# Performance work log

Hardware: AMD Instinct MI355X
Metric: run time of the kernel (lower is better)

## Reference

```python
import jax, jax.numpy as jnp
import numpy as np

D_LATENT = 128
WIDTH = 64
MODES = 32
N_LAYERS = 4
N_INST = 8
LIFT_L = 64   # lift_shape = (width, 64)
B = 128
OUT_LEN = 4096
EPS = 1e-5


def _gelu(x):
    return jax.nn.gelu(x, approximate=False)  # torch nn.GELU default = exact erf


def setup_inputs() -> dict:
    key = jax.random.key(0)
    ks = jax.random.split(key, 16)
    n = lambda k, shape, s=0.02: (s * jax.random.normal(k, shape)).astype(jnp.float32)
    spec_scale = 1.0 / (WIDTH * WIDTH)
    return {
        "z": jax.random.normal(ks[0], (B, D_LATENT), dtype=jnp.float32),
        "instrument_params": jax.random.normal(ks[1], (B, N_INST), dtype=jnp.float32),
        "lift_w": n(ks[2], (D_LATENT, WIDTH * LIFT_L)),
        "lift_b": jnp.zeros((WIDTH * LIFT_L,), jnp.float32),
        "inst_w1": n(ks[3], (N_INST, WIDTH), 0.3),
        "inst_b1": jnp.zeros((WIDTH,), jnp.float32),
        "inst_w2": n(ks[4], (WIDTH, WIDTH), 0.1),
        "inst_b2": jnp.zeros((WIDTH,), jnp.float32),
        "spec_w": (spec_scale * jax.random.normal(ks[5], (N_LAYERS, WIDTH, WIDTH, MODES, 2))).astype(jnp.float32),
        "pw_w": n(ks[6], (N_LAYERS, WIDTH, WIDTH), 0.1),   # (layer, out, in)
        "pw_b": jnp.zeros((N_LAYERS, WIDTH), jnp.float32),
        "proj_w1": n(ks[7], (2 * WIDTH, WIDTH), 0.1),      # (out, in)
        "proj_b1": jnp.zeros((2 * WIDTH,), jnp.float32),
        "proj_w2": n(ks[8], (1, 2 * WIDTH), 0.1),
        "proj_b2": jnp.zeros((1,), jnp.float32),
        "out_len": OUT_LEN,
    }


def _interp_linear(x, out_len):
    # torch F.interpolate(mode='linear', align_corners=False)
    in_len = x.shape[-1]
    src = jnp.clip((jnp.arange(out_len, dtype=x.dtype) + 0.5) * (in_len / out_len) - 0.5, 0.0, in_len - 1)
    i0 = jnp.floor(src).astype(jnp.int32)
    i1 = jnp.minimum(i0 + 1, in_len - 1)
    w = src - i0.astype(x.dtype)
    return x[..., i0] * (1.0 - w) + x[..., i1] * w


def _spectral_conv(x, w):
    # x: (B, C, L) real; w: (C_in, C_out, modes, 2)
    L = x.shape[-1]
    xf = jnp.fft.rfft(x, axis=-1)                 # (B, C, L//2+1) complex64
    xr = jnp.real(xf[:, :, :MODES])
    xi = jnp.imag(xf[:, :, :MODES])
    wr, wi = w[..., 0], w[..., 1]
    out_r = jnp.einsum('bim,iom->bom', xr, wr) - jnp.einsum('bim,iom->bom', xi, wi)
    out_i = jnp.einsum('bim,iom->bom', xr, wi) + jnp.einsum('bim,iom->bom', xi, wr)
    n_freq = L // 2 + 1
    of = (out_r + 1j * out_i).astype(xf.dtype)
    of = jnp.pad(of, ((0, 0), (0, 0), (0, n_freq - MODES)))
    return jnp.fft.irfft(of, n=L, axis=-1)


def reference(z, instrument_params, lift_w, lift_b, inst_w1, inst_b1, inst_w2, inst_b2,
              spec_w, pw_w, pw_b, proj_w1, proj_b1, proj_w2, proj_b2, out_len):
    Bz = z.shape[0]
    x = (z @ lift_w + lift_b).reshape(Bz, WIDTH, LIFT_L)
    x = _interp_linear(x, out_len)                              # (B, W, L)
    cond = _gelu(instrument_params @ inst_w1 + inst_b1) @ inst_w2 + inst_b2
    x = x + cond[:, :, None]
    for l in range(N_LAYERS):
        x1 = _spectral_conv(x, spec_w[l])
        x2 = jnp.einsum('bil,oi->bol', x, pw_w[l]) + pw_b[l][None, :, None]
        h = x1 + x2
        mu = h.mean(axis=-1, keepdims=True)
        var = h.var(axis=-1, keepdims=True)                     # biased, like InstanceNorm1d
        x = _gelu((h - mu) * jax.lax.rsqrt(var + EPS))
    h = _gelu(jnp.einsum('bil,oi->bol', x, proj_w1) + proj_b1[None, :, None])
    out = jnp.einsum('bil,oi->bol', h, proj_w2) + proj_b2[None, :, None]
    return out[:, 0, :]                                         # (B, out_len)
```

## Files before the change

### kernel.cpp

```cpp
#include <hip/hip_runtime.h>
#include <math.h>


typedef _Float16 half8 __attribute__((ext_vector_type(8)));
typedef __attribute__((ext_vector_type(4))) float fx4;

__device__ __forceinline__ float gelu_f(float x){
    float u = x*x;
    float a = x * fmaf(-0.1029443f, u, -2.3022083f);
    float e = exp2f(a);
    float r = __builtin_amdgcn_rcpf(1.0f + e);
    return x * r;
}
__device__ __forceinline__ unsigned short f2h(float f){
    union { _Float16 h; unsigned short u; } c;
    c.h = (_Float16)f;
    return c.u;
}
__device__ __forceinline__ float h2f(unsigned short u){
    union { unsigned short u; _Float16 h; } c;
    c.u = u;
    return (float)c.h;
}

static const size_t OFF_XH    = 0;
static const size_t OFF_XT    = 16777216;
static const size_t OFF_TABB  = 33554432;
static const size_t OFF_TABT  = 33685504;
static const size_t OFF_MAH   = 33816576;
static const size_t OFF_PWWH  = 34078720;
static const size_t OFF_W1H   = 34086912;
static const size_t OFF_COND  = 34091008;
static const size_t OFF_STATS = 34099200;
static const size_t OFF_DFTP  = 34115584;
static const size_t OFF_X0    = 38309888;

__global__ void k_tab(unsigned short* __restrict__ tabB, unsigned short* __restrict__ tabT,
                      const float* __restrict__ pww, unsigned short* __restrict__ pwwh,
                      const float* __restrict__ pj1w, unsigned short* __restrict__ w1h){
    int t = blockIdx.x*256 + threadIdx.x;
    if (t < 16384) pwwh[t] = f2h(pww[t]);
    if (t < 8192)  w1h[t]  = f2h(pj1w[t]);
    int m2 = t >> 12, n = t & 4095;
    int m = m2 & 31;
    int r = (m*n) & 4095;
    int r2 = (r >= 2048) ? (r - 4096) : r;
    float a = (float)r2 * 1.5339807878856412e-3f;
    float v = (m2 >= 32) ? sinf(a) : cosf(a);
    tabB[(size_t)m2*4096 + n] = f2h(v);
    tabT[(size_t)n*64 + m2]   = f2h(v * 0.015625f);
}

__global__ __launch_bounds__(64) void k_cond(const float* __restrict__ instp,
        const float* __restrict__ w1, const float* __restrict__ b1,
        const float* __restrict__ w2, const float* __restrict__ b2,
        float* __restrict__ cond){
    int b = blockIdx.x, tid = threadIdx.x;
    __shared__ float ipl[8];
    __shared__ float tl[64];
    if (tid < 8) ipl[tid] = instp[b*8 + tid];
    __syncthreads();
    float s = b1[tid];
    #pragma unroll
    for (int k = 0; k < 8; ++k) s = fmaf(ipl[k], w1[k*64 + tid], s);
    tl[tid] = gelu_f(s);
    __syncthreads();
    float c = b2[tid];
    #pragma unroll 8
    for (int j = 0; j < 64; ++j) c = fmaf(tl[j], w2[j*64 + tid], c);
    cond[b*64 + tid] = c;
}

__global__ __launch_bounds__(256) void k_liftc(const float* __restrict__ z,
        const float* __restrict__ lw, const float* __restrict__ lb,
        const float* __restrict__ cond, float* __restrict__ x0){
    int b = blockIdx.x, q = blockIdx.y;
    int t = threadIdx.x;
    __shared__ float zl[128];
    if (t < 128) zl[t] = z[b*128 + t];
    __syncthreads();
    #pragma unroll
    for (int i = 0; i < 4; ++i){
        int e = q*1024 + i*256 + t;
        float s = lb[e];
        #pragma unroll 8
        for (int d = 0; d < 128; ++d)
            s = fmaf(zl[d], lw[(size_t)d*4096 + e], s);
        x0[(size_t)b*4096 + e] = s + cond[b*64 + (e >> 6)];
    }
}

template<int MODE, int DODFT>
__global__ __launch_bounds__(256) void k_prep(
        const unsigned short* __restrict__ xhp, const float* __restrict__ statsr,
        const unsigned short* __restrict__ tabB, const float* __restrict__ x0,
        unsigned short* __restrict__ xT, float* __restrict__ dftp)
{
    int b = blockIdx.x, ng = blockIdx.y;
    int t = threadIdx.x;
    int w = t >> 6, lane = t & 63;
    int lrow = lane & 15, g = lane >> 4;
    __shared__ __align__(16) unsigned short xl[2][4096];
    __shared__ float xs[(MODE == 2) ? 65*64 : 1];
    int co = t >> 2, nq = t & 3;
    float mu = 0.f, rs = 1.f;
    if (MODE == 1){
        float2 sr = *(const float2*)(statsr + (size_t)(b*64+co)*2);
        mu = sr.x * (1.f/4096.f);
        float var = fmaf(sr.y, 1.f/4096.f, -mu*mu);
        rs = rsqrtf(var + 1e-5f);
    }
    if (MODE == 2){
        const float* xb0 = x0 + (size_t)b*4096;
        #pragma unroll
        for (int i = 0; i < 16; ++i){
            int idx = i*256 + t;
            xs[(idx >> 6)*65 + (idx & 63)] = xb0[idx];
        }
        __syncthreads();
    }
    fx4 acc[4];
    #pragma unroll
    for (int i = 0; i < 4; ++i) acc[i] = (fx4){0.f,0.f,0.f,0.f};

    const unsigned short* hrow = xhp + ((size_t)(b*64+co))*4096 + ng*512 + nq*16;
    unsigned short* xtbase = xT + ((size_t)b*4096 + (size_t)ng*512)*64;

    uint4 cA, cB;
    if (MODE == 1){ cA = *(const uint4*)(hrow); cB = *(const uint4*)(hrow + 8); }
    for (int it = 0; it < 8; ++it){
        int n0 = ng*512 + it*64;
        char* xb = (char*)(&xl[it & 1][0]);
        uint4 nA, nB;
        if (MODE == 1 && it < 7){
            nA = *(const uint4*)(hrow + (it+1)*64);
            nB = *(const uint4*)(hrow + (it+1)*64 + 8);
        }
        unsigned int pk[8];
        if (MODE == 1){
            unsigned int hu[8] = {cA.x,cA.y,cA.z,cA.w,cB.x,cB.y,cB.z,cB.w};
            #pragma unroll
            for (int i = 0; i < 8; ++i){
                float f0 = h2f((unsigned short)(hu[i] & 0xFFFFu));
                float f1 = h2f((unsigned short)(hu[i] >> 16));
                f0 = gelu_f((f0 - mu)*rs);
                f1 = gelu_f((f1 - mu)*rs);
                pk[i] = (unsigned int)f2h(f0) | ((unsigned int)f2h(f1) << 16);
            }
        } else {
            const float* xr = xs + co*65;
            #pragma unroll
            for (int i = 0; i < 8; ++i){
                float v[2];
                #pragma unroll
                for (int q = 0; q < 2; ++q){
                    int n = n0 + nq*16 + i*2 + q;
                    float src = (n + 0.5f)*0.015625f - 0.5f;
                    src = fminf(fmaxf(src, 0.0f), 63.0f);
                    int i0 = (int)src;
                    int i1 = (i0 + 1 > 63) ? 63 : (i0 + 1);
                    float wt = src - (float)i0;
                    v[q] = xr[i0] + wt*(xr[i1] - xr[i0]);
                }
                pk[i] = (unsigned int)f2h(v[0]) | ((unsigned int)f2h(v[1]) << 16);
            }
        }
        unsigned int base = (unsigned int)co*128 + (unsigned int)nq*32;
        unsigned int sw = (unsigned int)((co & 7) << 4);
        *(uint4*)(xb + ((base +  0) ^ sw)) = make_uint4(pk[0],pk[1],pk[2],pk[3]);
        *(uint4*)(xb + ((base + 16) ^ sw)) = make_uint4(pk[4],pk[5],pk[6],pk[7]);
        __syncthreads();

        if (DODFT){
            int m0 = w*16;
            #pragma unroll
            for (int ks = 0; ks < 2; ++ks){
                int kk = ks*32 + g*8;
                half8 af = *(const half8*)(tabB + (size_t)(m0 + lrow)*4096 + n0 + kk);
                #pragma unroll
                for (int ct = 0; ct < 4; ++ct){
                    int row = ct*16 + lrow;
                    unsigned int ba = ((unsigned int)row*128 + (unsigned int)kk*2)
                                      ^ (unsigned int)((row & 7) << 4);
                    half8 bf = *(const half8*)(xb + ba);
                    acc[ct] = __builtin_amdgcn_mfma_f32_16x16x32_f16(af, bf, acc[ct], 0, 0, 0);
                }
            }
        }
        {
            int n = t & 63, coq = t >> 6;
            unsigned int opk[8];
            #pragma unroll
            for (int i = 0; i < 8; ++i){
                int r0 = coq*16 + 2*i, r1 = r0 + 1;
                unsigned int a0 = ((unsigned int)r0*128 + (unsigned int)n*2)
                                  ^ (unsigned int)((r0 & 7) << 4);
                unsigned int a1 = ((unsigned int)r1*128 + (unsigned int)n*2)
                                  ^ (unsigned int)((r1 & 7) << 4);
                unsigned short v0 = *(const unsigned short*)(xb + a0);
                unsigned short v1 = *(const unsigned short*)(xb + a1);
                opk[i] = (unsigned int)v0 | ((unsigned int)v1 << 16);
            }
            unsigned short* dst = xtbase + (size_t)(it*64 + n)*64 + coq*16;
            *(uint4*)dst       = make_uint4(opk[0],opk[1],opk[2],opk[3]);
            *(uint4*)(dst + 8) = make_uint4(opk[4],opk[5],opk[6],opk[7]);
        }
        if (MODE == 1 && it < 7){ cA = nA; cB = nB; }
    }
    if (DODFT){
        int m0 = w*16;
        #pragma unroll
        for (int ct = 0; ct < 4; ++ct){
            float4 v = make_float4(acc[ct][0], acc[ct][1], acc[ct][2], acc[ct][3]);
            *(float4*)(dftp + ((size_t)(b*8+ng)*64 + ct*16 + lrow)*64 + m0 + g*4) = v;
        }
    }
}

__global__ __launch_bounds__(256) void k_mix(const float* __restrict__ dftp,
        const float* __restrict__ specw, unsigned short* __restrict__ mah,
        float* __restrict__ statsr, int l){
    int b = blockIdx.x, coq = blockIdx.y, t = threadIdx.x;
    __shared__ float xm[64*64];
    if (t < 128) statsr[b*128 + t] = 0.f;
    const float* dp = dftp + (size_t)b*8*4096;
    #pragma unroll
    for (int i = 0; i < 4; ++i){
        int e = i*1024 + t*4;
        float4 s = make_float4(0.f,0.f,0.f,0.f);
        #pragma unroll
        for (int ng = 0; ng < 8; ++ng){
            float4 v = *(const float4*)(dp + (size_t)ng*4096 + e);
            s.x += v.x; s.y += v.y; s.z += v.z; s.w += v.w;
        }
        if (e & 32){ s.x = -s.x; s.y = -s.y; s.z = -s.z; s.w = -s.w; }
        *(float4*)(xm + e) = s;
    }
    __syncthreads();
    int mq = t & 3, ciq = (t >> 2) & 3, co_l = t >> 4;
    int co = coq*16 + co_l;
    float yr[8] = {0,0,0,0,0,0,0,0}, yi[8] = {0,0,0,0,0,0,0,0};
    const float* wbase = specw + (size_t)l*262144 + (size_t)co*64 + mq*16;
    #pragma unroll 4
    for (int cil = 0; cil < 16; ++cil){
        int ci = ciq*16 + cil;
        const float* wp = wbase + (size_t)ci*4096;
        float4 w0 = *(const float4*)(wp);
        float4 w1v = *(const float4*)(wp + 4);
        float4 w2v = *(const float4*)(wp + 8);
        float4 w3v = *(const float4*)(wp + 12);
        const float* xc = xm + ci*64 + mq*8;
        float4 r0 = *(const float4*)(xc);
        float4 r1 = *(const float4*)(xc + 4);
        float4 i0 = *(const float4*)(xc + 32);
        float4 i1 = *(const float4*)(xc + 36);
        float wr[8] = {w0.x,w0.z,w1v.x,w1v.z,w2v.x,w2v.z,w3v.x,w3v.z};
        float wi[8] = {w0.y,w0.w,w1v.y,w1v.w,w2v.y,w2v.w,w3v.y,w3v.w};
        float xr[8] = {r0.x,r0.y,r0.z,r0.w,r1.x,r1.y,r1.z,r1.w};
        float xi[8] = {i0.x,i0.y,i0.z,i0.w,i1.x,i1.y,i1.z,i1.w};
        #pragma unroll
        for (int mm = 0; mm < 8; ++mm){
            yr[mm] = fmaf(xr[mm], wr[mm], fmaf(-xi[mm], wi[mm], yr[mm]));
            yi[mm] = fmaf(xr[mm], wi[mm], fmaf( xi[mm], wr[mm], yi[mm]));
        }
    }
    #pragma unroll
    for (int mm = 0; mm < 8; ++mm){
        yr[mm] += __shfl_xor(yr[mm], 4); yr[mm] += __shfl_xor(yr[mm], 8);
        yi[mm] += __shfl_xor(yi[mm], 4); yi[mm] += __shfl_xor(yi[mm], 8);
    }
    if (ciq == 0){
        unsigned short* mb = mah + (size_t)(b*64 + co)*64;
        unsigned int pr[4], pi[4];
        #pragma unroll
        for (int p = 0; p < 4; ++p){
            int m0 = mq*8 + 2*p;
            float s0 = (m0 == 0) ? 0.015625f : 0.03125f;
            pr[p] = (unsigned int)f2h(s0*yr[2*p]) | ((unsigned int)f2h(0.03125f*yr[2*p+1]) << 16);
            pi[p] = (unsigned int)f2h(-0.03125f*yi[2*p]) | ((unsigned int)f2h(-0.03125f*yi[2*p+1]) << 16);
        }
        *(uint4*)(mb + mq*8)      = make_uint4(pr[0],pr[1],pr[2],pr[3]);
        *(uint4*)(mb + 32 + mq*8) = make_uint4(pi[0],pi[1],pi[2],pi[3]);
    }
}

__global__ __launch_bounds__(256, 4) void k_pass3(
        const unsigned short* __restrict__ xT, const unsigned short* __restrict__ tabT,
        const unsigned short* __restrict__ pwwh, const float* __restrict__ pwb,
        const unsigned short* __restrict__ mah, unsigned short* __restrict__ xh,
        float* __restrict__ statsr, int lay)
{
    int b = blockIdx.x, ntg = blockIdx.y;
    int t = threadIdx.x, w = t >> 6, lane = t & 63;
    int lrow = lane & 15, g = lane >> 4;
    int nsl = ntg*256 + w*64;

    half8 A[4][4];
    #pragma unroll
    for (int nt = 0; nt < 4; ++nt){
        int n = nsl + nt*16 + lrow;
        #pragma unroll
        for (int ks = 0; ks < 4; ++ks){
            int k = ks*32 + g*8;
            const unsigned short* src = (k < 64)
                ? (xT   + ((size_t)b*4096 + n)*64 + k)
                : (tabT + (size_t)n*64 + (k - 64));
            A[nt][ks] = *(const half8*)src;
        }
    }
    __shared__ float sred[2][4][64];
    #pragma unroll
    for (int cot = 0; cot < 4; ++cot){
        int co = cot*16 + lrow;
        half8 Bv[4];
        #pragma unroll
        for (int ks = 0; ks < 4; ++ks){
            int k = ks*32 + g*8;
            const unsigned short* src = (k < 64)
                ? (pwwh + ((size_t)lay*64 + co)*64 + k)
                : (mah  + ((size_t)b*64 + co)*64 + (k - 64));
            Bv[ks] = *(const half8*)src;
        }
        fx4 acc[4];
        #pragma unroll
        for (int i = 0; i < 4; ++i) acc[i] = (fx4){0.f,0.f,0.f,0.f};
        #pragma unroll
        for (int ks = 0; ks < 4; ++ks)
            #pragma unroll
            for (int nt = 0; nt < 4; ++nt)
                acc[nt] = __builtin_amdgcn_mfma_f32_16x16x32_f16(A[nt][ks], Bv[ks], acc[nt], 0, 0, 0);

        float pb = pwb[lay*64 + co];
        unsigned short* hr = xh + ((size_t)(b*64+co))*4096;
        float sS = 0.f, sQ = 0.f;
        #pragma unroll
        for (int nt = 0; nt < 4; ++nt){
            float h0 = acc[nt][0] + pb;
            float h1 = acc[nt][1] + pb;
            float h2 = acc[nt][2] + pb;
            float h3 = acc[nt][3] + pb;
            uint2 pk;
            pk.x = (unsigned int)f2h(h0) | ((unsigned int)f2h(h1) << 16);
            pk.y = (unsigned int)f2h(h2) | ((unsigned int)f2h(h3) << 16);
            *(uint2*)(hr + nsl + nt*16 + g*4) = pk;
            sS += (h0 + h1) + (h2 + h3);
            float q = h0*h0;
            q = fmaf(h1, h1, q); q = fmaf(h2, h2, q); q = fmaf(h3, h3, q);
            sQ += q;
        }
        sS += __shfl_xor(sS, 16); sQ += __shfl_xor(sQ, 16);
        sS += __shfl_xor(sS, 32); sQ += __shfl_xor(sQ, 32);
        if (g == 0){
            sred[0][w][cot*16 + lrow] = sS;
            sred[1][w][cot*16 + lrow] = sQ;
        }
    }
    __syncthreads();
    if (t < 64){
        float S = 0.f, Q = 0.f;
        #pragma unroll
        for (int ww = 0; ww < 4; ++ww){ S += sred[0][ww][t]; Q += sred[1][ww][t]; }
        atomicAdd(statsr + (size_t)(b*64+t)*2,     S);
        atomicAdd(statsr + (size_t)(b*64+t)*2 + 1, Q);
    }
}

__global__ __launch_bounds__(256) void k_proj2(
        const unsigned short* __restrict__ xhp, const float* __restrict__ statsr,
        const unsigned short* __restrict__ w1h, const float* __restrict__ b1,
        const float* __restrict__ w2, const float* __restrict__ b2,
        float* __restrict__ out)
{
    int b = blockIdx.x, ng = blockIdx.y;
    int t = threadIdx.x, w = t >> 6, lane = t & 63;
    int lrow = lane & 15, g = lane >> 4;
    int o2h = w & 1, nhalf = w >> 1;
    __shared__ __align__(16) unsigned short xl[2][4096];
    __shared__ float sred[2][2][2][2][16];

    int ci = t >> 2, nq = t & 3;
    float2 sr = *(const float2*)(statsr + (size_t)(b*64+ci)*2);
    float mu = sr.x * (1.f/4096.f);
    float var = fmaf(sr.y, 1.f/4096.f, -mu*mu);
    float rs = rsqrtf(var + 1e-5f);
    const unsigned short* hrow = xhp + ((size_t)(b*64+ci))*4096 + ng*512 + nq*16;

    half8 A[4][2];
    #pragma unroll
    for (int ot = 0; ot < 4; ++ot)
        #pragma unroll
        for (int ks = 0; ks < 2; ++ks)
            A[ot][ks] = *(const half8*)(w1h + (size_t)(o2h*64 + ot*16 + lrow)*64 + ks*32 + g*8);
    float bb[16], wv[16];
    #pragma unroll
    for (int ot = 0; ot < 4; ++ot)
        #pragma unroll
        for (int j = 0; j < 4; ++j){
            int o2 = o2h*64 + ot*16 + g*4 + j;
            bb[ot*4+j] = b1[o2];
            wv[ot*4+j] = w2[o2];
        }
    float bias2 = b2[0];

    uint4 cA = *(const uint4*)(hrow);
    uint4 cB = *(const uint4*)(hrow + 8);
    for (int it = 0; it < 8; ++it){
        char* xb = (char*)(&xl[it & 1][0]);
        uint4 nA, nB;
        if (it < 7){
            nA = *(const uint4*)(hrow + (it+1)*64);
            nB = *(const uint4*)(hrow + (it+1)*64 + 8);
        }
        unsigned int pk[8];
        {
            unsigned int hu[8] = {cA.x,cA.y,cA.z,cA.w,cB.x,cB.y,cB.z,cB.w};
            #pragma unroll
            for (int i = 0; i < 8; ++i){
                float f0 = h2f((unsigned short)(hu[i] & 0xFFFFu));
                float f1 = h2f((unsigned short)(hu[i] >> 16));
                f0 = gelu_f((f0 - mu)*rs);
                f1 = gelu_f((f1 - mu)*rs);
                pk[i] = (unsigned int)f2h(f0) | ((unsigned int)f2h(f1) << 16);
            }
        }
        unsigned int base = (unsigned int)ci*128 + (unsigned int)nq*32;
        unsigned int sw = (unsigned int)((ci & 7) << 4);
        *(uint4*)(xb + ((base +  0) ^ sw)) = make_uint4(pk[0],pk[1],pk[2],pk[3]);
        *(uint4*)(xb + ((base + 16) ^ sw)) = make_uint4(pk[4],pk[5],pk[6],pk[7]);
        __syncthreads();

        if (it > 0 && t < 64){
            int nh = t >> 5, rem = t & 31, ntf = rem >> 4, cl = rem & 15;
            out[(size_t)b*4096 + ng*512 + (it-1)*64 + t] =
                sred[(it-1)&1][nh][ntf][0][cl] + sred[(it-1)&1][nh][ntf][1][cl] + bias2;
        }

        #pragma unroll
        for (int nt = 0; nt < 2; ++nt){
            int n_l = nhalf*32 + nt*16 + lrow;
            half8 Bf[2];
            #pragma unroll
            for (int ks = 0; ks < 2; ++ks){
                union { unsigned short u[8]; half8 v; } bu;
                #pragma unroll
                for (int e = 0; e < 8; ++e){
                    int cie = ks*32 + g*8 + e;
                    unsigned int ba = ((unsigned int)cie*128 + (unsigned int)n_l*2)
                                      ^ (unsigned int)((cie & 7) << 4);
                    bu.u[e] = *(const unsigned short*)(xb + ba);
                }
                Bf[ks] = bu.v;
            }
            fx4 acc[4];
            #pragma unroll
            for (int i = 0; i < 4; ++i) acc[i] = (fx4){0.f,0.f,0.f,0.f};
            #pragma unroll
            for (int ks = 0; ks < 2; ++ks)
                #pragma unroll
                for (int ot = 0; ot < 4; ++ot)
                    acc[ot] = __builtin_amdgcn_mfma_f32_16x16x32_f16(A[ot][ks], Bf[ks], acc[ot], 0, 0, 0);
            float p = 0.f;
            #pragma unroll
            for (int ot = 0; ot < 4; ++ot)
                #pragma unroll
                for (int j = 0; j < 4; ++j)
                    p = fmaf(wv[ot*4+j], gelu_f(acc[ot][j] + bb[ot*4+j]), p);
            p += __shfl_xor(p, 16); p += __shfl_xor(p, 32);
            if (lane < 16) sred[it & 1][nhalf][nt][o2h][lane] = p;
        }
        if (it < 7){ cA = nA; cB = nB; }
    }
    __syncthreads();
    if (t < 64){
        int nh = t >> 5, rem = t & 31, ntf = rem >> 4, cl = rem & 15;
        out[(size_t)b*4096 + ng*512 + 7*64 + t] =
            sred[1][nh][ntf][0][cl] + sred[1][nh][ntf][1][cl] + bias2;
    }
}

extern "C" void kernel_launch(void* const* d_in, const int* in_sizes, int n_in,
                              void* d_out, int out_size, void* d_ws, size_t ws_size,
                              hipStream_t stream) {
    (void)in_sizes; (void)n_in; (void)out_size; (void)ws_size;
    const float* z      = (const float*)d_in[0];
    const float* instp  = (const float*)d_in[1];
    const float* lift_w = (const float*)d_in[2];
    const float* lift_b = (const float*)d_in[3];
    const float* iw1    = (const float*)d_in[4];
    const float* ib1    = (const float*)d_in[5];
    const float* iw2    = (const float*)d_in[6];
    const float* ib2    = (const float*)d_in[7];
    const float* specw  = (const float*)d_in[8];
    const float* pww    = (const float*)d_in[9];
    const float* pwb    = (const float*)d_in[10];
    const float* pj1w   = (const float*)d_in[11];
    const float* pj1b   = (const float*)d_in[12];
    const float* pj2w   = (const float*)d_in[13];
    const float* pj2b   = (const float*)d_in[14];

    float* ws = (float*)d_ws;
    unsigned short* xh    = (unsigned short*)(ws + OFF_XH);
    unsigned short* xT    = (unsigned short*)(ws + OFF_XT);
    unsigned short* tabB  = (unsigned short*)(ws + OFF_TABB);
    unsigned short* tabT  = (unsigned short*)(ws + OFF_TABT);
    unsigned short* mah   = (unsigned short*)(ws + OFF_MAH);
    unsigned short* pwwh  = (unsigned short*)(ws + OFF_PWWH);
    unsigned short* w1h   = (unsigned short*)(ws + OFF_W1H);
    float* cond   = ws + OFF_COND;
    float* statsr = ws + OFF_STATS;
    float* dftp   = ws + OFF_DFTP;
    float* x0     = ws + OFF_X0;
    float* out    = (float*)d_out;

    k_tab  <<<dim3(1024),  dim3(256), 0, stream>>>(tabB, tabT, pww, pwwh, pj1w, w1h);
    k_cond <<<dim3(128),   dim3(64),  0, stream>>>(instp, iw1, ib1, iw2, ib2, cond);
    k_liftc<<<dim3(128,4), dim3(256), 0, stream>>>(z, lift_w, lift_b, cond, x0);

    for (int l = 0; l < 4; ++l){
        if (l == 0)
            k_prep<2,1><<<dim3(128,8), dim3(256), 0, stream>>>(xh, statsr, tabB, x0, xT, dftp);
        else
            k_prep<1,1><<<dim3(128,8), dim3(256), 0, stream>>>(xh, statsr, tabB, x0, xT, dftp);
        k_mix  <<<dim3(128,4),  dim3(256), 0, stream>>>(dftp, specw, mah, statsr, l);
        k_pass3<<<dim3(128,16), dim3(256), 0, stream>>>(xT, tabT, pwwh, pwb, mah, xh, statsr, l);
    }
    k_proj2<<<dim3(128,8), dim3(256), 0, stream>>>(xh, statsr, w1h, pj1b, pj2w, pj2b, out);
}
```

Baseline: 442.3 us.

## Recompute normalized activations in pass3 instead of storing transposed xT buffer

The prep kernel no longer writes a transposed fp16 copy of the activations (xT). The pointwise/inverse-DFT kernel now reads the raw pre-norm activations itself, applies instance norm and GELU (or the lift interpolation on layer 0), and transposes through LDS before the MFMA. Stats are double-buffered so pass3 can read the previous layer's stats while accumulating new ones. The projection kernel also gets an LDS transpose so its B fragments load as vectors instead of scalar gathers. This removes a large global write and read per layer, at the cost of redundant GELU work, extra barriers, fewer blocks (grid 16→8 in y) and lower occupancy hints.

Result: faster. 420.1 us, median of 2 (-5.0%).

```diff
diff --git a/kernel.cpp b/kernel.cpp
--- a/kernel.cpp
+++ b/kernel.cpp
@@ -23,17 +23,17 @@
     return (float)c.h;
 }
 
-static const size_t OFF_XH    = 0;
-static const size_t OFF_XT    = 16777216;
-static const size_t OFF_TABB  = 33554432;
-static const size_t OFF_TABT  = 33685504;
-static const size_t OFF_MAH   = 33816576;
-static const size_t OFF_PWWH  = 34078720;
-static const size_t OFF_W1H   = 34086912;
-static const size_t OFF_COND  = 34091008;
-static const size_t OFF_STATS = 34099200;
-static const size_t OFF_DFTP  = 34115584;
-static const size_t OFF_X0    = 38309888;
+static const size_t OFF_XH     = 0;
+static const size_t OFF_TABB   = 33554432;
+static const size_t OFF_TABT   = 33685504;
+static const size_t OFF_MAH    = 33816576;
+static const size_t OFF_PWWH   = 34078720;
+static const size_t OFF_W1H    = 34086912;
+static const size_t OFF_COND   = 34091008;
+static const size_t OFF_STATS  = 34099200;
+static const size_t OFF_DFTP   = 34115584;
+static const size_t OFF_X0     = 38309888;
+static const size_t OFF_STATS2 = 38834176;
 
 __global__ void k_tab(unsigned short* __restrict__ tabB, unsigned short* __restrict__ tabT,
                       const float* __restrict__ pww, unsigned short* __restrict__ pwwh,
@@ -90,11 +90,11 @@
     }
 }
 
-template<int MODE, int DODFT>
+template<int MODE>
 __global__ __launch_bounds__(256) void k_prep(
-        const unsigned short* __restrict__ xhp, const float* __restrict__ statsr,
+        const unsigned short* __restrict__ xhp, const float* __restrict__ statsIn,
         const unsigned short* __restrict__ tabB, const float* __restrict__ x0,
-        unsigned short* __restrict__ xT, float* __restrict__ dftp)
+        float* __restrict__ dftp)
 {
     int b = blockIdx.x, ng = blockIdx.y;
     int t = threadIdx.x;
@@ -102,10 +102,10 @@
     int lrow = lane & 15, g = lane >> 4;
     __shared__ __align__(16) unsigned short xl[2][4096];
     __shared__ float xs[(MODE == 2) ? 65*64 : 1];
-    int co = t >> 2, nq = t & 3;
+    int ci = t >> 2, nq = t & 3;
     float mu = 0.f, rs = 1.f;
     if (MODE == 1){
-        float2 sr = *(const float2*)(statsr + (size_t)(b*64+co)*2);
+        float2 sr = *(const float2*)(statsIn + (size_t)(b*64+ci)*2);
         mu = sr.x * (1.f/4096.f);
         float var = fmaf(sr.y, 1.f/4096.f, -mu*mu);
         rs = rsqrtf(var + 1e-5f);
@@ -123,8 +123,7 @@
     #pragma unroll
     for (int i = 0; i < 4; ++i) acc[i] = (fx4){0.f,0.f,0.f,0.f};
 
-    const unsigned short* hrow = xhp + ((size_t)(b*64+co))*4096 + ng*512 + nq*16;
-    unsigned short* xtbase = xT + ((size_t)b*4096 + (size_t)ng*512)*64;
+    const unsigned short* hrow = xhp + ((size_t)(b*64+ci))*4096 + ng*512 + nq*16;
 
     uint4 cA, cB;
     if (MODE == 1){ cA = *(const uint4*)(hrow); cB = *(const uint4*)(hrow + 8); }
@@ -148,7 +147,7 @@
                 pk[i] = (unsigned int)f2h(f0) | ((unsigned int)f2h(f1) << 16);
             }
         } else {
-            const float* xr = xs + co*65;
+            const float* xr = xs + ci*65;
             #pragma unroll
             for (int i = 0; i < 8; ++i){
                 float v[2];
@@ -165,13 +164,13 @@
                 pk[i] = (unsigned int)f2h(v[0]) | ((unsigned int)f2h(v[1]) << 16);
             }
         }
-        unsigned int base = (unsigned int)co*128 + (unsigned int)nq*32;
-        unsigned int sw = (unsigned int)((co & 7) << 4);
+        unsigned int base = (unsigned int)ci*128 + (unsigned int)nq*32;
+        unsigned int sw = (unsigned int)((ci & 7) << 4);
         *(uint4*)(xb + ((base +  0) ^ sw)) = make_uint4(pk[0],pk[1],pk[2],pk[3]);
         *(uint4*)(xb + ((base + 16) ^ sw)) = make_uint4(pk[4],pk[5],pk[6],pk[7]);
         __syncthreads();
 
-        if (DODFT){
+        {
             int m0 = w*16;
             #pragma unroll
             for (int ks = 0; ks < 2; ++ks){
@@ -187,27 +186,9 @@
                 }
             }
         }
-        {
-            int n = t & 63, coq = t >> 6;
-            unsigned int opk[8];
-            #pragma unroll
-            for (int i = 0; i < 8; ++i){
-                int r0 = coq*16 + 2*i, r1 = r0 + 1;
-                unsigned int a0 = ((unsigned int)r0*128 + (unsigned int)n*2)
-                                  ^ (unsigned int)((r0 & 7) << 4);
-                unsigned int a1 = ((unsigned int)r1*128 + (unsigned int)n*2)
-                                  ^ (unsigned int)((r1 & 7) << 4);
-                unsigned short v0 = *(const unsigned short*)(xb + a0);
-                unsigned short v1 = *(const unsigned short*)(xb + a1);
-                opk[i] = (unsigned int)v0 | ((unsigned int)v1 << 16);
-            }
-            unsigned short* dst = xtbase + (size_t)(it*64 + n)*64 + coq*16;
-            *(uint4*)dst       = make_uint4(opk[0],opk[1],opk[2],opk[3]);
-            *(uint4*)(dst + 8) = make_uint4(opk[4],opk[5],opk[6],opk[7]);
-        }
         if (MODE == 1 && it < 7){ cA = nA; cB = nB; }
     }
-    if (DODFT){
+    {
         int m0 = w*16;
         #pragma unroll
         for (int ct = 0; ct < 4; ++ct){
@@ -219,10 +200,10 @@
 
 __global__ __launch_bounds__(256) void k_mix(const float* __restrict__ dftp,
         const float* __restrict__ specw, unsigned short* __restrict__ mah,
-        float* __restrict__ statsr, int l){
+        float* __restrict__ statsZero, int l){
     int b = blockIdx.x, coq = blockIdx.y, t = threadIdx.x;
     __shared__ float xm[64*64];
-    if (t < 128) statsr[b*128 + t] = 0.f;
+    if (t < 128) statsZero[b*128 + t] = 0.f;
     const float* dp = dftp + (size_t)b*8*4096;
     #pragma unroll
     for (int i = 0; i < 4; ++i){
@@ -284,42 +265,133 @@
     }
 }
 
-__global__ __launch_bounds__(256, 4) void k_pass3(
-        const unsigned short* __restrict__ xT, const unsigned short* __restrict__ tabT,
+template<int MODE>
+__global__ __launch_bounds__(256, 2) void k_pass3(
+        const unsigned short* __restrict__ xhp, const float* __restrict__ statsIn,
+        const float* __restrict__ x0, const unsigned short* __restrict__ tabT,
         const unsigned short* __restrict__ pwwh, const float* __restrict__ pwb,
         const unsigned short* __restrict__ mah, unsigned short* __restrict__ xh,
-        float* __restrict__ statsr, int lay)
+        float* __restrict__ statsOut, int lay)
 {
-    int b = blockIdx.x, ntg = blockIdx.y;
+    int b = blockIdx.x, ng = blockIdx.y;
     int t = threadIdx.x, w = t >> 6, lane = t & 63;
     int lrow = lane & 15, g = lane >> 4;
-    int nsl = ntg*256 + w*64;
-
-    half8 A[4][4];
-    #pragma unroll
-    for (int nt = 0; nt < 4; ++nt){
-        int n = nsl + nt*16 + lrow;
-        #pragma unroll
-        for (int ks = 0; ks < 4; ++ks){
-            int k = ks*32 + g*8;
-            const unsigned short* src = (k < 64)
-                ? (xT   + ((size_t)b*4096 + n)*64 + k)
-                : (tabT + (size_t)n*64 + (k - 64));
-            A[nt][ks] = *(const half8*)src;
-        }
-    }
+    __shared__ __align__(16) unsigned short xl1[4096];
+    __shared__ __align__(16) unsigned short xl2[4096];
+    __shared__ float xs[(MODE == 2) ? 65*64 : 1];
     __shared__ float sred[2][4][64];
+
+    int ci = t >> 2, nq = t & 3;
+    float mu = 0.f, rs = 1.f;
+    if (MODE == 1){
+        float2 sr = *(const float2*)(statsIn + (size_t)(b*64+ci)*2);
+        mu = sr.x * (1.f/4096.f);
+        float var = fmaf(sr.y, 1.f/4096.f, -mu*mu);
+        rs = rsqrtf(var + 1e-5f);
+    }
+    if (MODE == 2){
+        const float* xb0 = x0 + (size_t)b*4096;
+        #pragma unroll
+        for (int i = 0; i < 16; ++i){
+            int idx = i*256 + t;
+            xs[(idx >> 6)*65 + (idx & 63)] = xb0[idx];
+        }
+        __syncthreads();
+    }
+    half8 Bv[4][4];
     #pragma unroll
     for (int cot = 0; cot < 4; ++cot){
         int co = cot*16 + lrow;
-        half8 Bv[4];
         #pragma unroll
         for (int ks = 0; ks < 4; ++ks){
             int k = ks*32 + g*8;
             const unsigned short* src = (k < 64)
                 ? (pwwh + ((size_t)lay*64 + co)*64 + k)
                 : (mah  + ((size_t)b*64 + co)*64 + (k - 64));
-            Bv[ks] = *(const half8*)src;
+            Bv[cot][ks] = *(const half8*)src;
+        }
+    }
+    float pb[4];
+    #pragma unroll
+    for (int cot = 0; cot < 4; ++cot) pb[cot] = pwb[lay*64 + cot*16 + lrow];
+    float sS[4] = {0,0,0,0}, sQ[4] = {0,0,0,0};
+
+    const unsigned short* hrow = xhp + ((size_t)(b*64+ci))*4096 + ng*512 + nq*16;
+    uint4 cA, cB;
+    if (MODE == 1){ cA = *(const uint4*)(hrow); cB = *(const uint4*)(hrow + 8); }
+
+    for (int it = 0; it < 8; ++it){
+        int n0 = ng*512 + it*64;
+        uint4 nA, nB;
+        if (MODE == 1 && it < 7){
+            nA = *(const uint4*)(hrow + (it+1)*64);
+            nB = *(const uint4*)(hrow + (it+1)*64 + 8);
+        }
+        unsigned int pk[8];
+        if (MODE == 1){
+            unsigned int hu[8] = {cA.x,cA.y,cA.z,cA.w,cB.x,cB.y,cB.z,cB.w};
+            #pragma unroll
+            for (int i = 0; i < 8; ++i){
+                float f0 = h2f((unsigned short)(hu[i] & 0xFFFFu));
+                float f1 = h2f((unsigned short)(hu[i] >> 16));
+                f0 = gelu_f((f0 - mu)*rs);
+                f1 = gelu_f((f1 - mu)*rs);
+                pk[i] = (unsigned int)f2h(f0) | ((unsigned int)f2h(f1) << 16);
+            }
+        } else {
+            const float* xr = xs + ci*65;
+            #pragma unroll
+            for (int i = 0; i < 8; ++i){
+                float v[2];
+                #pragma unroll
+                for (int q = 0; q < 2; ++q){
+                    int n = n0 + nq*16 + i*2 + q;
+                    float src = (n + 0.5f)*0.015625f - 0.5f;
+                    src = fminf(fmaxf(src, 0.0f), 63.0f);
+                    int i0 = (int)src;
+                    int i1 = (i0 + 1 > 63) ? 63 : (i0 + 1);
+                    float wt = src - (float)i0;
+                    v[q] = xr[i0] + wt*(xr[i1] - xr[i0]);
+                }
+                pk[i] = (unsigned int)f2h(v[0]) | ((unsigned int)f2h(v[1]) << 16);
+            }
+        }
+        unsigned int base = (unsigned int)ci*128 + (unsigned int)nq*32;
+        unsigned int sw = (unsigned int)((ci & 7) << 4);
+        *(uint4*)((char*)xl1 + ((base +  0) ^ sw)) = make_uint4(pk[0],pk[1],pk[2],pk[3]);
+        *(uint4*)((char*)xl1 + ((base + 16) ^ sw)) = make_uint4(pk[4],pk[5],pk[6],pk[7]);
+        __syncthreads();
+
+        {
+            int n = t & 63, coq = t >> 6;
+            unsigned int opk[8];
+            #pragma unroll
+            for (int i = 0; i < 8; ++i){
+                int r0 = coq*16 + 2*i, r1 = r0 + 1;
+                unsigned int a0 = ((unsigned int)r0*128 + (unsigned int)n*2)
+                                  ^ (unsigned int)((r0 & 7) << 4);
+                unsigned int a1 = ((unsigned int)r1*128 + (unsigned int)n*2)
+                                  ^ (unsigned int)((r1 & 7) << 4);
+                unsigned short v0 = *(const unsigned short*)((const char*)xl1 + a0);
+                unsigned short v1 = *(const unsigned short*)((const char*)xl1 + a1);
+                opk[i] = (unsigned int)v0 | ((unsigned int)v1 << 16);
+            }
+            unsigned int b0 = (unsigned int)n*128 + (unsigned int)coq*32;
+            unsigned int swn = (unsigned int)((n & 7) << 4);
+            *(uint4*)((char*)xl2 + ((b0 +  0) ^ swn)) = make_uint4(opk[0],opk[1],opk[2],opk[3]);
+            *(uint4*)((char*)xl2 + ((b0 + 16) ^ swn)) = make_uint4(opk[4],opk[5],opk[6],opk[7]);
+        }
+        __syncthreads();
+
+        int nl = w*16 + lrow;
+        unsigned int swa = (unsigned int)((nl & 7) << 4);
+        half8 Af[4];
+        Af[0] = *(const half8*)((const char*)xl2 + (((unsigned int)nl*128 +  0 + g*16) ^ swa));
+        Af[1] = *(const half8*)((const char*)xl2 + (((unsigned int)nl*128 + 64 + g*16) ^ swa));
+        {
+            const unsigned short* tb = tabT + (size_t)(n0 + nl)*64 + g*8;
+            Af[2] = *(const half8*)(tb);
+            Af[3] = *(const half8*)(tb + 32);
         }
         fx4 acc[4];
         #pragma unroll
@@ -327,32 +399,36 @@
         #pragma unroll
         for (int ks = 0; ks < 4; ++ks)
             #pragma unroll
-            for (int nt = 0; nt < 4; ++nt)
-                acc[nt] = __builtin_amdgcn_mfma_f32_16x16x32_f16(A[nt][ks], Bv[ks], acc[nt], 0, 0, 0);
-
-        float pb = pwb[lay*64 + co];
-        unsigned short* hr = xh + ((size_t)(b*64+co))*4096;
-        float sS = 0.f, sQ = 0.f;
-        #pragma unroll
-        for (int nt = 0; nt < 4; ++nt){
-            float h0 = acc[nt][0] + pb;
-            float h1 = acc[nt][1] + pb;
-            float h2 = acc[nt][2] + pb;
-            float h3 = acc[nt][3] + pb;
-            uint2 pk;
-            pk.x = (unsigned int)f2h(h0) | ((unsigned int)f2h(h1) << 16);
-            pk.y = (unsigned int)f2h(h2) | ((unsigned int)f2h(h3) << 16);
-            *(uint2*)(hr + nsl + nt*16 + g*4) = pk;
-            sS += (h0 + h1) + (h2 + h3);
+            for (int cot = 0; cot < 4; ++cot)
+                acc[cot] = __builtin_amdgcn_mfma_f32_16x16x32_f16(Af[ks], Bv[cot][ks], acc[cot], 0, 0, 0);
+
+        #pragma unroll
+        for (int cot = 0; cot < 4; ++cot){
+            int co = cot*16 + lrow;
+            unsigned short* hr = xh + ((size_t)(b*64+co))*4096;
+            float h0 = acc[cot][0] + pb[cot];
+            float h1 = acc[cot][1] + pb[cot];
+            float h2 = acc[cot][2] + pb[cot];
+            float h3 = acc[cot][3] + pb[cot];
+            uint2 pk2;
+            pk2.x = (unsigned int)f2h(h0) | ((unsigned int)f2h(h1) << 16);
+            pk2.y = (unsigned int)f2h(h2) | ((unsigned int)f2h(h3) << 16);
+            *(uint2*)(hr + n0 + w*16 + g*4) = pk2;
+            sS[cot] += (h0 + h1) + (h2 + h3);
             float q = h0*h0;
             q = fmaf(h1, h1, q); q = fmaf(h2, h2, q); q = fmaf(h3, h3, q);
-            sQ += q;
-        }
-        sS += __shfl_xor(sS, 16); sQ += __shfl_xor(sQ, 16);
-        sS += __shfl_xor(sS, 32); sQ += __shfl_xor(sQ, 32);
+            sQ[cot] += q;
+        }
+        if (MODE == 1 && it < 7){ cA = nA; cB = nB; }
+    }
+    #pragma unroll
+    for (int cot = 0; cot < 4; ++cot){
+        float s = sS[cot], q = sQ[cot];
+        s += __shfl_xor(s, 16); q += __shfl_xor(q, 16);
+        s += __shfl_xor(s, 32); q += __shfl_xor(q, 32);
         if (g == 0){
-            sred[0][w][cot*16 + lrow] = sS;
-            sred[1][w][cot*16 + lrow] = sQ;
+            sred[0][w][cot*16 + lrow] = s;
+            sred[1][w][cot*16 + lrow] = q;
         }
     }
     __syncthreads();
@@ -360,13 +436,13 @@
         float S = 0.f, Q = 0.f;
         #pragma unroll
         for (int ww = 0; ww < 4; ++ww){ S += sred[0][ww][t]; Q += sred[1][ww][t]; }
-        atomicAdd(statsr + (size_t)(b*64+t)*2,     S);
-        atomicAdd(statsr + (size_t)(b*64+t)*2 + 1, Q);
+        atomicAdd(statsOut + (size_t)(b*64+t)*2,     S);
+        atomicAdd(statsOut + (size_t)(b*64+t)*2 + 1, Q);
     }
 }
 
 __global__ __launch_bounds__(256) void k_proj2(
-        const unsigned short* __restrict__ xhp, const float* __restrict__ statsr,
+        const unsigned short* __restrict__ xhp, const float* __restrict__ statsIn,
         const unsigned short* __restrict__ w1h, const float* __restrict__ b1,
         const float* __restrict__ w2, const float* __restrict__ b2,
         float* __restrict__ out)
@@ -375,11 +451,12 @@
     int t = threadIdx.x, w = t >> 6, lane = t & 63;
     int lrow = lane & 15, g = lane >> 4;
     int o2h = w & 1, nhalf = w >> 1;
-    __shared__ __align__(16) unsigned short xl[2][4096];
+    __shared__ __align__(16) unsigned short xl1[4096];
+    __shared__ __align__(16) unsigned short xl2[4096];
     __shared__ float sred[2][2][2][2][16];
 
     int ci = t >> 2, nq = t & 3;
-    float2 sr = *(const float2*)(statsr + (size_t)(b*64+ci)*2);
+    float2 sr = *(const float2*)(statsIn + (size_t)(b*64+ci)*2);
     float mu = sr.x * (1.f/4096.f);
     float var = fmaf(sr.y, 1.f/4096.f, -mu*mu);
     float rs = rsqrtf(var + 1e-5f);
@@ -405,7 +482,6 @@
     uint4 cA = *(const uint4*)(hrow);
     uint4 cB = *(const uint4*)(hrow + 8);
     for (int it = 0; it < 8; ++it){
-        char* xb = (char*)(&xl[it & 1][0]);
         uint4 nA, nB;
         if (it < 7){
             nA = *(const uint4*)(hrow + (it+1)*64);
@@ -425,8 +501,29 @@
         }
         unsigned int base = (unsigned int)ci*128 + (unsigned int)nq*32;
         unsigned int sw = (unsigned int)((ci & 7) << 4);
-        *(uint4*)(xb + ((base +  0) ^ sw)) = make_uint4(pk[0],pk[1],pk[2],pk[3]);
-        *(uint4*)(xb + ((base + 16) ^ sw)) = make_uint4(pk[4],pk[5],pk[6],pk[7]);
+        *(uint4*)((char*)xl1 + ((base +  0) ^ sw)) = make_uint4(pk[0],pk[1],pk[2],pk[3]);
+        *(uint4*)((char*)xl1 + ((base + 16) ^ sw)) = make_uint4(pk[4],pk[5],pk[6],pk[7]);
+        __syncthreads();
+
+        {
+            int n = t & 63, coq = t >> 6;
+            unsigned int opk[8];
+            #pragma unroll
+            for (int i = 0; i < 8; ++i){
+                int r0 = coq*16 + 2*i, r1 = r0 + 1;
+                unsigned int a0 = ((unsigned int)r0*128 + (unsigned int)n*2)
+                                  ^ (unsigned int)((r0 & 7) << 4);
+                unsigned int a1 = ((unsigned int)r1*128 + (unsigned int)n*2)
+                                  ^ (unsigned int)((r1 & 7) << 4);
+                unsigned short v0 = *(const unsigned short*)((const char*)xl1 + a0);
+                unsigned short v1 = *(const unsigned short*)((const char*)xl1 + a1);
+                opk[i] = (unsigned int)v0 | ((unsigned int)v1 << 16);
+            }
+            unsigned int b0 = (unsigned int)n*128 + (unsigned int)coq*32;
+            unsigned int swn = (unsigned int)((n & 7) << 4);
+            *(uint4*)((char*)xl2 + ((b0 +  0) ^ swn)) = make_uint4(opk[0],opk[1],opk[2],opk[3]);
+            *(uint4*)((char*)xl2 + ((b0 + 16) ^ swn)) = make_uint4(opk[4],opk[5],opk[6],opk[7]);
+        }
         __syncthreads();
 
         if (it > 0 && t < 64){
@@ -438,19 +535,10 @@
         #pragma unroll
         for (int nt = 0; nt < 2; ++nt){
             int n_l = nhalf*32 + nt*16 + lrow;
+            unsigned int swa = (unsigned int)((n_l & 7) << 4);
             half8 Bf[2];
-            #pragma unroll
-            for (int ks = 0; ks < 2; ++ks){
-                union { unsigned short u[8]; half8 v; } bu;
-                #pragma unroll
-                for (int e = 0; e < 8; ++e){
-                    int cie = ks*32 + g*8 + e;
-                    unsigned int ba = ((unsigned int)cie*128 + (unsigned int)n_l*2)
-                                      ^ (unsigned int)((cie & 7) << 4);
-                    bu.u[e] = *(const unsigned short*)(xb + ba);
-                }
-                Bf[ks] = bu.v;
-            }
+            Bf[0] = *(const half8*)((const char*)xl2 + (((unsigned int)n_l*128 +  0 + g*16) ^ swa));
+            Bf[1] = *(const half8*)((const char*)xl2 + (((unsigned int)n_l*128 + 64 + g*16) ^ swa));
             fx4 acc[4];
             #pragma unroll
             for (int i = 0; i < 4; ++i) acc[i] = (fx4){0.f,0.f,0.f,0.f};
@@ -500,16 +588,15 @@
 
     float* ws = (float*)d_ws;
     unsigned short* xh    = (unsigned short*)(ws + OFF_XH);
-    unsigned short* xT    = (unsigned short*)(ws + OFF_XT);
     unsigned short* tabB  = (unsigned short*)(ws + OFF_TABB);
     unsigned short* tabT  = (unsigned short*)(ws + OFF_TABT);
     unsigned short* mah   = (unsigned short*)(ws + OFF_MAH);
     unsigned short* pwwh  = (unsigned short*)(ws + OFF_PWWH);
     unsigned short* w1h   = (unsigned short*)(ws + OFF_W1H);
     float* cond   = ws + OFF_COND;
-    float* statsr = ws + OFF_STATS;
     float* dftp   = ws + OFF_DFTP;
     float* x0     = ws + OFF_X0;
+    float* sbuf[2] = { ws + OFF_STATS, ws + OFF_STATS2 };
     float* out    = (float*)d_out;
 
     k_tab  <<<dim3(1024),  dim3(256), 0, stream>>>(tabB, tabT, pww, pwwh, pj1w, w1h);
@@ -517,12 +604,17 @@
     k_liftc<<<dim3(128,4), dim3(256), 0, stream>>>(z, lift_w, lift_b, cond, x0);
 
     for (int l = 0; l < 4; ++l){
+        float* sIn  = sbuf[l & 1];
+        float* sOut = sbuf[(l + 1) & 1];
         if (l == 0)
-            k_prep<2,1><<<dim3(128,8), dim3(256), 0, stream>>>(xh, statsr, tabB, x0, xT, dftp);
+            k_prep<2><<<dim3(128,8), dim3(256), 0, stream>>>(xh, sIn, tabB, x0, dftp);
         else
-            k_prep<1,1><<<dim3(128,8), dim3(256), 0, stream>>>(xh, statsr, tabB, x0, xT, dftp);
-        k_mix  <<<dim3(128,4),  dim3(256), 0, stream>>>(dftp, specw, mah, statsr, l);
-        k_pass3<<<dim3(128,16), dim3(256), 0, stream>>>(xT, tabT, pwwh, pwb, mah, xh, statsr, l);
-    }
-    k_proj2<<<dim3(128,8), dim3(256), 0, stream>>>(xh, statsr, w1h, pj1b, pj2w, pj2b, out);
-}
+            k_prep<1><<<dim3(128,8), dim3(256), 0, stream>>>(xh, sIn, tabB, x0, dftp);
+        k_mix<<<dim3(128,4), dim3(256), 0, stream>>>(dftp, specw, mah, sOut, l);
+        if (l == 0)
+            k_pass3<2><<<dim3(128,8), dim3(256), 0, stream>>>(xh, sIn, x0, tabT, pwwh, pwb, mah, xh, sOut, l);
+        else
+            k_pass3<1><<<dim3(128,8), dim3(256), 0, stream>>>(xh, sIn, x0, tabT, pwwh, pwb, mah, xh, sOut, l);
+    }
+    k_proj2<<<dim3(128,8), dim3(256), 0, stream>>>(xh, sbuf[0], w1h, pj1b, pj2w, pj2b, out);
+}
```
